# Performance work log

Measured on AMD Instinct MI355X. Metric: run time of the kernel, lower is better.

## Reference

```python
import jax, jax.numpy as jnp
import numpy as np

N, H, W = 131072, 28, 28


def _mute(x):
    """Vectorized mute_bit: m,e = frexp(x); e = 0 if e > 1 else e; ldexp(m, e).
    Equivalent to scaling x by 2**(-e) when e > 1, identity otherwise.
    frexp's integer exponent carries no gradient, so this is also vjp-safe."""
    e = jnp.frexp(x)[1]                      # integer exponent, frexp convention: x = m * 2**e, m in [0.5,1)
    shift = jnp.where(e > 1, -e, 0).astype(x.dtype)
    return x * jnp.exp2(shift)


def setup_inputs() -> dict:
    key = jax.random.key(0)
    kx, = jax.random.split(key, 1)
    # scale by 8 so a substantial fraction of elements have exponent > 1 (mute path fires)
    x = jax.random.normal(kx, (N, H, W), dtype=jnp.float32) * 8.0
    rows = jnp.array([0, 7, 14, 21], dtype=jnp.int32)
    cols = jnp.array([3, 10, 17, 24], dtype=jnp.int32)
    return {"x": x, "rows": rows, "cols": cols}


def reference(x, rows, cols):
    # Mute selected full rows first (X[i][r][j] for j in 0..27), then selected full cols
    # (X[i][j][c] for j in 0..27) on the already-updated array, matching loop order.
    x = x.at[:, rows, :].set(_mute(x[:, rows, :]))
    x = x.at[:, :, cols].set(_mute(x[:, :, cols]))
    return x
```

## Files before the change

kernel.cpp:

```cpp
#include <hip/hip_runtime.h>

__device__ __forceinline__ float mute1(float v, unsigned on) {
    unsigned b = __float_as_uint(v);
    float m = __uint_as_float((b & 0x807FFFFFu) | 0x3F000000u);
    return (on && ((b & 0x7F800000u) >= 0x40000000u)) ? m : v;
}

typedef float f32x4 __attribute__((ext_vector_type(4)));

__device__ __forceinline__ f32x4 mute4(f32x4 v, unsigned sel) {
    v.x = mute1(v.x, sel & 1u);
    v.y = mute1(v.y, sel & 2u);
    v.z = mute1(v.z, sel & 4u);
    v.w = mute1(v.w, sel & 8u);
    return v;
}

__device__ __forceinline__ unsigned sel_for(unsigned q, unsigned row_mask, unsigned col_mask) {
    unsigned h = q / 7u;
    unsigned w = (q - h * 7u) * 4u;
    return (((row_mask >> h) & 1u) ? 0xFu : 0u) | ((col_mask >> w) & 0xFu);
}

__global__ __launch_bounds__(256, 4) void mute_kernel(
    const f32x4* __restrict__ x, f32x4* __restrict__ out,
    const int* __restrict__ rows, const int* __restrict__ cols, int n4)
{
    unsigned row_mask = (1u << rows[0]) | (1u << rows[1]) | (1u << rows[2]) | (1u << rows[3]);
    unsigned col_mask = (1u << cols[0]) | (1u << cols[1]) | (1u << cols[2]) | (1u << cols[3]);

    const int stride = (int)(gridDim.x * 256u);
    int i = (int)(blockIdx.x * 256u + threadIdx.x);

    constexpr int U = 7;
    for (; i + (U - 1) * stride < n4; i += U * stride) {
        f32x4 v[U];
        #pragma unroll
        for (int u = 0; u < U; ++u)
            v[u] = __builtin_nontemporal_load(&x[i + u * stride]);
        #pragma unroll
        for (int u = 0; u < U; ++u) {
            unsigned q = (unsigned)(i + u * stride) % 196u;
            v[u] = mute4(v[u], sel_for(q, row_mask, col_mask));
        }
        #pragma unroll
        for (int u = 0; u < U; ++u)
            __builtin_nontemporal_store(v[u], &out[i + u * stride]);
    }
    for (; i < n4; i += stride) {
        unsigned q = (unsigned)i % 196u;
        __builtin_nontemporal_store(
            mute4(__builtin_nontemporal_load(&x[i]), sel_for(q, row_mask, col_mask)),
            &out[i]);
    }
}

extern "C" void kernel_launch(void* const* d_in, const int* in_sizes, int n_in,
                              void* d_out, int out_size, void* d_ws, size_t ws_size,
                              hipStream_t stream) {
    const float* x   = (const float*)d_in[0];
    const int* rows  = (const int*)d_in[1];
    const int* cols  = (const int*)d_in[2];
    float* out       = (float*)d_out;

    int n  = in_sizes[0];
    int n4 = n / 4;

    int blocks = 2048;
    int max_needed = (n4 + 255) / 256;
    if (blocks > max_needed) blocks = max_needed;

    mute_kernel<<<blocks, 256, 0, stream>>>(
        (const f32x4*)x, (f32x4*)out, rows, cols, n4);
}
```

Measured before the change: 661.6 us.

## Replace grid-stride loop with one-chunk-per-block launch and plain loads

Result: faster. 647.7 us (-2.1%).

```diff
diff --git a/kernel.cpp b/kernel.cpp
--- a/kernel.cpp
+++ b/kernel.cpp
@@ -6,9 +6,7 @@
     return (on && ((b & 0x7F800000u) >= 0x40000000u)) ? m : v;
 }
 
-typedef float f32x4 __attribute__((ext_vector_type(4)));
-
-__device__ __forceinline__ f32x4 mute4(f32x4 v, unsigned sel) {
+__device__ __forceinline__ float4 mute4(float4 v, unsigned sel) {
     v.x = mute1(v.x, sel & 1u);
     v.y = mute1(v.y, sel & 2u);
     v.z = mute1(v.z, sel & 4u);
@@ -22,36 +20,38 @@
     return (((row_mask >> h) & 1u) ? 0xFu : 0u) | ((col_mask >> w) & 0xFu);
 }
 
-__global__ __launch_bounds__(256, 4) void mute_kernel(
-    const f32x4* __restrict__ x, f32x4* __restrict__ out,
+constexpr int U = 7;
+
+__global__ __launch_bounds__(256) void mute_kernel(
+    const float4* __restrict__ x, float4* __restrict__ out,
     const int* __restrict__ rows, const int* __restrict__ cols, int n4)
 {
     unsigned row_mask = (1u << rows[0]) | (1u << rows[1]) | (1u << rows[2]) | (1u << rows[3]);
     unsigned col_mask = (1u << cols[0]) | (1u << cols[1]) | (1u << cols[2]) | (1u << cols[3]);
 
-    const int stride = (int)(gridDim.x * 256u);
-    int i = (int)(blockIdx.x * 256u + threadIdx.x);
+    int base = (int)(blockIdx.x * (256u * U) + threadIdx.x);
 
-    constexpr int U = 7;
-    for (; i + (U - 1) * stride < n4; i += U * stride) {
-        f32x4 v[U];
+    if (base + (U - 1) * 256 < n4) {
+        float4 v[U];
         #pragma unroll
         for (int u = 0; u < U; ++u)
-            v[u] = __builtin_nontemporal_load(&x[i + u * stride]);
+            v[u] = x[base + u * 256];
         #pragma unroll
         for (int u = 0; u < U; ++u) {
-            unsigned q = (unsigned)(i + u * stride) % 196u;
+            unsigned q = (unsigned)(base + u * 256) % 196u;
             v[u] = mute4(v[u], sel_for(q, row_mask, col_mask));
         }
         #pragma unroll
         for (int u = 0; u < U; ++u)
-            __builtin_nontemporal_store(v[u], &out[i + u * stride]);
-    }
-    for (; i < n4; i += stride) {
-        unsigned q = (unsigned)i % 196u;
-        __builtin_nontemporal_store(
-            mute4(__builtin_nontemporal_load(&x[i]), sel_for(q, row_mask, col_mask)),
-            &out[i]);
+            out[base + u * 256] = v[u];
+    } else {
+        for (int u = 0; u < U; ++u) {
+            int i = base + u * 256;
+            if (i < n4) {
+                unsigned q = (unsigned)i % 196u;
+                out[i] = mute4(x[i], sel_for(q, row_mask, col_mask));
+            }
+        }
     }
 }
 
@@ -66,10 +66,9 @@
     int n  = in_sizes[0];
     int n4 = n / 4;
 
-    int blocks = 2048;
-    int max_needed = (n4 + 255) / 256;
-    if (blocks > max_needed) blocks = max_needed;
+    int chunk  = 256 * U;
+    int blocks = (n4 + chunk - 1) / chunk;
 
     mute_kernel<<<blocks, 256, 0, stream>>>(
-        (const f32x4*)x, (f32x4*)out, rows, cols, n4);
+        (const float4*)x, (float4*)out, rows, cols, n4);
 }
```
